# Kernel optimization log

Hardware: AMD Instinct MI355X
Metric: run time of the kernel (lower is better)

The kernel has to match this reference:

```python
import jax, jax.numpy as jnp
import numpy as np
from jax.scipy.special import erf

N = 100000
PATCH = 10           # cells per dim: covers 2*nsigma*sigma_max / spacing <= 9
SPACING = (0.5, 0.5, 0.5)
NSIGMA = 3.0


def setup_inputs() -> dict:
    key = jax.random.key(0)
    k1, k2, k3, k4 = jax.random.split(key, 4)
    # sigma in [0.25, 0.75] distance units = [0.5, 1.5] x grid spacing
    sigma = 0.25 + 0.5 * jax.random.uniform(k1, (N, 3), dtype=jnp.float32)
    time = jax.random.uniform(k2, (N,), dtype=jnp.float32) * 10.0
    charge = jax.random.uniform(k3, (N,), dtype=jnp.float32) * 1000.0
    tail = jax.random.normal(k4, (N, 3), dtype=jnp.float32) * 20.0
    grid_spacing = jnp.asarray(SPACING, dtype=jnp.float32)
    nsigma = jnp.asarray(NSIGMA, dtype=jnp.float32)
    return {"sigma": sigma, "time": time, "charge": charge, "tail": tail,
            "grid_spacing": grid_spacing, "nsigma": nsigma}


def _transform(point, time):
    # pdims=(1,2), tdim=-1: new = [point[:,1], point[:,2], time]
    return jnp.stack([point[:, 1], point[:, 2], time], axis=-1)


def _raster_depos(grid_spacing, center, sigma, charge, nsigma):
    # center, sigma: [N,3]; returns rasters [N,P,P,P], offsets [N,3] int32
    imin = jnp.floor((center - nsigma * sigma) / grid_spacing)   # [N,3]
    offsets = imin.astype(jnp.int32)
    k = jnp.arange(PATCH + 1, dtype=center.dtype)                # cell edges index
    edges = (imin[:, :, None] + k) * grid_spacing[None, :, None]  # [N,3,P+1]
    z = (edges - center[:, :, None]) / (jnp.sqrt(2.0).astype(center.dtype) * sigma[:, :, None])
    cdf = 0.5 * (1.0 + erf(z))                                   # [N,3,P+1]
    w = cdf[..., 1:] - cdf[..., :-1]                             # [N,3,P] per-dim cell integrals
    rasters = (charge[:, None, None, None]
               * w[:, 0, :, None, None]
               * w[:, 1, None, :, None]
               * w[:, 2, None, None, :])                         # [N,P,P,P]
    return rasters, offsets


def reference(sigma, time, charge, tail, grid_spacing, nsigma):
    center = _transform(tail, time)
    rasters, offsets = _raster_depos(grid_spacing, center, sigma, charge, nsigma)
    return rasters, offsets
```

## Files before the change

### kernel.cpp

```cpp
#include <hip/hip_runtime.h>
#include <hip/hip_bf16.h>

#define PATCH 10
#define CELLS 1000
#define DPB   16

typedef float vfloat4 __attribute__((ext_vector_type(4)));

__global__ __launch_bounds__(512) void raster_kernel(
    const float* __restrict__ sigma,
    const float* __restrict__ time,
    const float* __restrict__ charge,
    const float* __restrict__ tail,
    const float* __restrict__ gs,
    const float* __restrict__ nsig,
    float* __restrict__ out_r,
    float* __restrict__ out_off,
    int n)
{
    const int d0  = blockIdx.x * DPB;
    const int tid = threadIdx.x;

    __shared__ float wq[DPB][32];

    if (tid < DPB * 30) {
        const int d   = tid / 30;
        const int r   = tid % 30;
        const int dim = r / 10;
        const int k   = r % 10;
        const int depo = d0 + d;
        if (depo < n) {
            float c;
            if (dim == 0)      c = tail[depo * 3 + 1];
            else if (dim == 1) c = tail[depo * 3 + 2];
            else               c = time[depo];
            const float sg = sigma[depo * 3 + dim];
            const float sp = gs[dim];
            const float ns = nsig[0];
            const float imin = floorf((c - ns * sg) / sp);
            const float inv  = 1.0f / (1.41421356237309f * sg);
            const float e0 = (imin + (float)k) * sp;
            const float e1 = (imin + (float)(k + 1)) * sp;
            const float cdf0 = 0.5f * (1.0f + erff((e0 - c) * inv));
            const float cdf1 = 0.5f * (1.0f + erff((e1 - c) * inv));
            wq[d][dim * 10 + k] = cdf1 - cdf0;
            if (k == 0) {
                out_off[(size_t)depo * 3 + dim] = (float)(int)imin;
                if (dim == 0) wq[d][30] = charge[depo];
            }
        }
    }
    __syncthreads();

    if (tid < 500) {
        const int half = (tid >= 250) ? 1 : 0;
        const int c4   = tid - 250 * half;
        const int cell0 = c4 * 4;

        int a0[4], a1[4], a2[4];
#pragma unroll
        for (int c = 0; c < 4; ++c) {
            const int cell = cell0 + c;
            a0[c] = cell / 100;
            a1[c] = 10 + (cell / 10) % 10;
            a2[c] = 20 + cell % 10;
        }

#pragma unroll
        for (int it = 0; it < DPB / 2; ++it) {
            const int d    = it * 2 + half;
            const int depo = d0 + d;
            if (depo < n) {
                const float q = wq[d][30];
                vfloat4 v;
                v.x = q * wq[d][a0[0]] * wq[d][a1[0]] * wq[d][a2[0]];
                v.y = q * wq[d][a0[1]] * wq[d][a1[1]] * wq[d][a2[1]];
                v.z = q * wq[d][a0[2]] * wq[d][a1[2]] * wq[d][a2[2]];
                v.w = q * wq[d][a0[3]] * wq[d][a1[3]] * wq[d][a2[3]];
                vfloat4* dst = reinterpret_cast<vfloat4*>(out_r + (size_t)depo * CELLS) + c4;
                __builtin_nontemporal_store(v, dst);
            }
        }
    }
}

extern "C" void kernel_launch(void* const* d_in, const int* in_sizes, int n_in,
                              void* d_out, int out_size, void* d_ws, size_t ws_size,
                              hipStream_t stream) {
    const float* sigma  = (const float*)d_in[0];
    const float* time_  = (const float*)d_in[1];
    const float* charge = (const float*)d_in[2];
    const float* tail   = (const float*)d_in[3];
    const float* gs     = (const float*)d_in[4];
    const float* nsig   = (const float*)d_in[5];

    const int n = in_sizes[1];

    float* out_r   = (float*)d_out;
    float* out_off = (float*)d_out + (size_t)n * CELLS;

    const int grid = (n + DPB - 1) / DPB;
    raster_kernel<<<grid, 512, 0, stream>>>(sigma, time_, charge, tail, gs, nsig,
                                            out_r, out_off, n);
}
```

Measured before the change: 81.55 us.

## Use persistent grid-stride blocks with double-buffered weights and prefetched inputs

```diff
diff --git a/kernel.cpp b/kernel.cpp
--- a/kernel.cpp
+++ b/kernel.cpp
@@ -1,13 +1,13 @@
 #include <hip/hip_runtime.h>
 #include <hip/hip_bf16.h>
 
-#define PATCH 10
 #define CELLS 1000
 #define DPB   16
+#define NTH   512
 
 typedef float vfloat4 __attribute__((ext_vector_type(4)));
 
-__global__ __launch_bounds__(512) void raster_kernel(
+__global__ __launch_bounds__(NTH) void raster_kernel(
     const float* __restrict__ sigma,
     const float* __restrict__ time,
     const float* __restrict__ charge,
@@ -16,71 +16,99 @@
     const float* __restrict__ nsig,
     float* __restrict__ out_r,
     float* __restrict__ out_off,
-    int n)
+    int n, int ngroups)
 {
-    const int d0  = blockIdx.x * DPB;
     const int tid = threadIdx.x;
 
-    __shared__ float wq[DPB][32];
+    __shared__ float wq[2][DPB][32];
 
-    if (tid < DPB * 30) {
-        const int d   = tid / 30;
-        const int r   = tid % 30;
-        const int dim = r / 10;
-        const int k   = r % 10;
-        const int depo = d0 + d;
+    const bool p1     = (tid < DPB * 30);
+    const int  p1_d   = tid / 30;
+    const int  p1_r   = tid - p1_d * 30;
+    const int  p1_dim = p1_r / 10;
+    const int  p1_k   = p1_r - p1_dim * 10;
+
+    const bool st   = (tid < 500);
+    const int  half = (tid >= 250) ? 1 : 0;
+    const int  c4   = tid - 250 * half;
+    int a0[4], a1[4], a2[4];
+#pragma unroll
+    for (int c = 0; c < 4; ++c) {
+        const int cell = c4 * 4 + c;
+        a0[c] = cell / 100;
+        a1[c] = 10 + (cell / 10) % 10;
+        a2[c] = 20 + cell % 10;
+    }
+
+    const float ns = nsig[0];
+    const float sp = p1 ? gs[p1_dim] : 0.5f;
+
+    float c_nx = 0.f, sg_nx = 1.f, q_nx = 0.f;
+    int g = blockIdx.x;
+    if (p1 && g < ngroups) {
+        const int depo = g * DPB + p1_d;
         if (depo < n) {
-            float c;
-            if (dim == 0)      c = tail[depo * 3 + 1];
-            else if (dim == 1) c = tail[depo * 3 + 2];
-            else               c = time[depo];
-            const float sg = sigma[depo * 3 + dim];
-            const float sp = gs[dim];
-            const float ns = nsig[0];
-            const float imin = floorf((c - ns * sg) / sp);
-            const float inv  = 1.0f / (1.41421356237309f * sg);
-            const float e0 = (imin + (float)k) * sp;
-            const float e1 = (imin + (float)(k + 1)) * sp;
-            const float cdf0 = 0.5f * (1.0f + erff((e0 - c) * inv));
-            const float cdf1 = 0.5f * (1.0f + erff((e1 - c) * inv));
-            wq[d][dim * 10 + k] = cdf1 - cdf0;
-            if (k == 0) {
-                out_off[(size_t)depo * 3 + dim] = (float)(int)imin;
-                if (dim == 0) wq[d][30] = charge[depo];
+            c_nx  = (p1_dim == 0) ? tail[depo * 3 + 1]
+                  : (p1_dim == 1) ? tail[depo * 3 + 2]
+                  : time[depo];
+            sg_nx = sigma[depo * 3 + p1_dim];
+            if (p1_r == 0) q_nx = charge[depo];
+        }
+    }
+
+    int buf = 0;
+    for (; g < ngroups; g += gridDim.x) {
+        if (p1) {
+            const int depo = g * DPB + p1_d;
+            if (depo < n) {
+                const float imin = floorf((c_nx - ns * sg_nx) / sp);
+                const float inv  = 1.0f / (1.41421356237309f * sg_nx);
+                const float e0   = (imin + (float)p1_k) * sp;
+                const float e1   = e0 + sp;
+                const float cdf0 = 0.5f * (1.0f + erff((e0 - c_nx) * inv));
+                const float cdf1 = 0.5f * (1.0f + erff((e1 - c_nx) * inv));
+                wq[buf][p1_d][p1_dim * 10 + p1_k] = cdf1 - cdf0;
+                if (p1_k == 0) {
+                    out_off[(size_t)depo * 3 + p1_dim] = (float)(int)imin;
+                    if (p1_dim == 0) wq[buf][p1_d][30] = q_nx;
+                }
             }
         }
-    }
-    __syncthreads();
+        asm volatile("s_waitcnt lgkmcnt(0)" ::: "memory");
+        __builtin_amdgcn_s_barrier();
+        asm volatile("" ::: "memory");
 
-    if (tid < 500) {
-        const int half = (tid >= 250) ? 1 : 0;
-        const int c4   = tid - 250 * half;
-        const int cell0 = c4 * 4;
-
-        int a0[4], a1[4], a2[4];
-#pragma unroll
-        for (int c = 0; c < 4; ++c) {
-            const int cell = cell0 + c;
-            a0[c] = cell / 100;
-            a1[c] = 10 + (cell / 10) % 10;
-            a2[c] = 20 + cell % 10;
+        const int gn = g + gridDim.x;
+        if (p1 && gn < ngroups) {
+            const int depo = gn * DPB + p1_d;
+            if (depo < n) {
+                c_nx  = (p1_dim == 0) ? tail[depo * 3 + 1]
+                      : (p1_dim == 1) ? tail[depo * 3 + 2]
+                      : time[depo];
+                sg_nx = sigma[depo * 3 + p1_dim];
+                if (p1_r == 0) q_nx = charge[depo];
+            }
         }
 
+        if (st) {
 #pragma unroll
-        for (int it = 0; it < DPB / 2; ++it) {
-            const int d    = it * 2 + half;
-            const int depo = d0 + d;
-            if (depo < n) {
-                const float q = wq[d][30];
-                vfloat4 v;
-                v.x = q * wq[d][a0[0]] * wq[d][a1[0]] * wq[d][a2[0]];
-                v.y = q * wq[d][a0[1]] * wq[d][a1[1]] * wq[d][a2[1]];
-                v.z = q * wq[d][a0[2]] * wq[d][a1[2]] * wq[d][a2[2]];
-                v.w = q * wq[d][a0[3]] * wq[d][a1[3]] * wq[d][a2[3]];
-                vfloat4* dst = reinterpret_cast<vfloat4*>(out_r + (size_t)depo * CELLS) + c4;
-                __builtin_nontemporal_store(v, dst);
+            for (int it = 0; it < DPB / 2; ++it) {
+                const int d    = it * 2 + half;
+                const int depo = g * DPB + d;
+                if (depo < n) {
+                    const float q = wq[buf][d][30];
+                    vfloat4 v;
+                    v.x = q * wq[buf][d][a0[0]] * wq[buf][d][a1[0]] * wq[buf][d][a2[0]];
+                    v.y = q * wq[buf][d][a0[1]] * wq[buf][d][a1[1]] * wq[buf][d][a2[1]];
+                    v.z = q * wq[buf][d][a0[2]] * wq[buf][d][a1[2]] * wq[buf][d][a2[2]];
+                    v.w = q * wq[buf][d][a0[3]] * wq[buf][d][a1[3]] * wq[buf][d][a2[3]];
+                    vfloat4* dst =
+                        reinterpret_cast<vfloat4*>(out_r + (size_t)depo * CELLS) + c4;
+                    __builtin_nontemporal_store(v, dst);
+                }
             }
         }
+        buf ^= 1;
     }
 }
 
@@ -99,7 +127,8 @@
     float* out_r   = (float*)d_out;
     float* out_off = (float*)d_out + (size_t)n * CELLS;
 
-    const int grid = (n + DPB - 1) / DPB;
-    raster_kernel<<<grid, 512, 0, stream>>>(sigma, time_, charge, tail, gs, nsig,
-                                            out_r, out_off, n);
+    const int ngroups = (n + DPB - 1) / DPB;
+    int grid = ngroups < 1024 ? ngroups : 1024;
+    raster_kernel<<<grid, NTH, 0, stream>>>(sigma, time_, charge, tail, gs, nsig,
+                                            out_r, out_off, n, ngroups);
 }
```

Result: slower. 85.14 us (+4.4%).
